# Kernel tuning notes

Measured on AMD Instinct MI355X. Metric: run time of the kernel, lower is better.

Reference implementation:

```python
import jax, jax.numpy as jnp
import numpy as np

# NMS hyperparameters (from init_kwargs / standard detection settings)
CONF_THRESH = 0.05
NMS_THRESH = 0.5
MAX_PER_CLASS = 200
MAX_PER_IMAGE = 100
PRE_NMS_TOPK = 1000  # standard pre-NMS per-class candidate cap


def setup_inputs() -> dict:
    key = jax.random.key(0)
    k1, k2, k3 = jax.random.split(key, 3)
    N, C = 20000, 80
    # per-anchor per-class confidences in [0, 1]
    scores = jax.random.uniform(k1, (1, N, C), dtype=jnp.float32)
    # well-formed boxes (x1, y1, x2, y2) in normalized coords
    centers = jax.random.uniform(k2, (N, 2), dtype=jnp.float32)
    wh = jax.random.uniform(k3, (N, 2), dtype=jnp.float32) * 0.2 + 0.01
    boxes = jnp.concatenate([centers - wh / 2, centers + wh / 2], axis=-1)  # [N, 4]
    return {"scores": scores, "boxes": boxes}


def reference(scores, boxes):
    """Multiclass NMS: confidence threshold -> per-class greedy IoU suppression
    (max_per_class kept) -> global top-max_per_image. Returns kept scores
    (fixed shape [MAX_PER_IMAGE], zero-padded), matching the wrapper which
    returns the selected scores."""
    cls_scores_all = scores[0].T  # [C, N]
    j = jnp.arange(PRE_NMS_TOPK)

    def nms_one_class(cls_scores):  # [N] -> [MAX_PER_CLASS]
        top_s, idx = jax.lax.top_k(cls_scores, PRE_NMS_TOPK)  # [K]
        b = boxes[idx]  # [K, 4]
        x1, y1, x2, y2 = b[:, 0], b[:, 1], b[:, 2], b[:, 3]
        area = (x2 - x1) * (y2 - y1)  # [K]
        # pairwise IoU [K, K]
        iw = jnp.clip(jnp.minimum(x2[:, None], x2[None, :]) - jnp.maximum(x1[:, None], x1[None, :]), 0.0)
        ih = jnp.clip(jnp.minimum(y2[:, None], y2[None, :]) - jnp.maximum(y1[:, None], y1[None, :]), 0.0)
        inter = iw * ih
        iou = inter / (area[:, None] + area[None, :] - inter + 1e-9)
        valid = top_s > CONF_THRESH  # confidence threshold

        def body(i, keep):
            # if box i survives, suppress later boxes with IoU above threshold
            sup = keep[i] & (iou[i] > NMS_THRESH) & (j > i)
            return keep & ~sup

        keep = jax.lax.fori_loop(0, PRE_NMS_TOPK, body, valid)
        kept = jnp.where(keep, top_s, 0.0)
        return jax.lax.top_k(kept, MAX_PER_CLASS)[0]  # cap per class

    per_class = jax.vmap(nms_one_class)(cls_scores_all)  # [C, MAX_PER_CLASS]
    # global cap: top max_per_image scores across all classes
    return jax.lax.top_k(per_class.reshape(-1), MAX_PER_IMAGE)[0]
```

## Files before the change

kernel.cpp:

```cpp
#include <hip/hip_runtime.h>
#include <stdint.h>

#define N_DET 20000
#define N_CLS 80
#define NELEM (N_DET * N_CLS)
#define TOPK  1000
#define CONF  0.05f
#define CANDS 1280
#define SORTN 2048
#define NBLK  128

typedef unsigned long long u64;
typedef unsigned int u32;

__device__ __forceinline__ bool iou_gt_half(float4 bi, float ai,
                                            float4 bj, float aj) {
  #pragma clang fp contract(off)
  float iw = fmaxf(fminf(bi.z, bj.z) - fmaxf(bi.x, bj.x), 0.0f);
  float ih = fmaxf(fminf(bi.w, bj.w) - fmaxf(bi.y, bj.y), 0.0f);
  float inter = iw * ih;
  float denom = ai + aj - inter + 1e-9f;
  return (double)inter * 33554432.0 > (double)denom * 16777217.0;
}

#define OFF_T16    0
#define OFF_CNT    960
#define OFF_CLSOUT 641280
#define OFF_GHA    682240
#define OFF_GHB    723200
#define OFF_CAND   805120
#define OFF_BCNT   1624320

__global__ __launch_bounds__(256) void k_zero(u32* __restrict__ gh) {
  uint4 z4 = make_uint4(0u, 0u, 0u, 0u);
  uint4* p = (uint4*)gh;
  int i = blockIdx.x * 256 + threadIdx.x;
  if (i < 7680) p[i] = z4;
}

__global__ __launch_bounds__(256) void k_histA(
    const float* __restrict__ S, u32* __restrict__ gh) {
  __shared__ u32 h[N_CLS * 129];
  for (int i = threadIdx.x; i < N_CLS * 129; i += 256) h[i] = 0;
  __syncthreads();
  const int per = NELEM / 4 / NBLK;
  const float4* S4 = (const float4*)S;
  const int v0 = blockIdx.x * per;
  for (int v = v0 + threadIdx.x; v < v0 + per; v += 256) {
    float4 f = S4[v];
    int c0 = (v * 4) % N_CLS;
    u32 b0 = __float_as_uint(f.x) >> 23; if (b0 > 127u) b0 = 127u;
    u32 b1 = __float_as_uint(f.y) >> 23; if (b1 > 127u) b1 = 127u;
    u32 b2 = __float_as_uint(f.z) >> 23; if (b2 > 127u) b2 = 127u;
    u32 b3 = __float_as_uint(f.w) >> 23; if (b3 > 127u) b3 = 127u;
    atomicAdd(&h[(c0 + 0) * 129 + b0], 1u);
    atomicAdd(&h[(c0 + 1) * 129 + b1], 1u);
    atomicAdd(&h[(c0 + 2) * 129 + b2], 1u);
    atomicAdd(&h[(c0 + 3) * 129 + b3], 1u);
  }
  __syncthreads();
  for (int i = threadIdx.x; i < N_CLS * 128; i += 256) {
    u32 v = h[(i >> 7) * 129 + (i & 127)];
    if (v) atomicAdd(&gh[i], v);
  }
}

__global__ __launch_bounds__(256) void k_histB_f(
    const float* __restrict__ S, const u32* __restrict__ ghA,
    u32* __restrict__ ghB) {
  __shared__ u32 h[N_CLS * 257];
  __shared__ u32 pA[N_CLS];
  for (int i = threadIdx.x; i < N_CLS * 128; i += 256)
    h[(i >> 7) * 129 + (i & 127)] = ghA[i];
  __syncthreads();
  if (threadIdx.x < N_CLS) {
    const int c = threadIdx.x;
    u32 acc = 0; u32 pref = 0;
    for (int b = 127; b >= 0; --b) {
      acc += h[c * 129 + b];
      if (acc >= TOPK) { pref = (u32)b; break; }
    }
    pA[c] = pref;
  }
  __syncthreads();
  for (int i = threadIdx.x; i < N_CLS * 257; i += 256) h[i] = 0;
  __syncthreads();
  const int per = NELEM / 4 / NBLK;
  const float4* S4 = (const float4*)S;
  const int v0 = blockIdx.x * per;
  for (int v = v0 + threadIdx.x; v < v0 + per; v += 256) {
    float4 f = S4[v];
    int c0 = (v * 4) % N_CLS;
    u32 bb[4] = {__float_as_uint(f.x), __float_as_uint(f.y),
                 __float_as_uint(f.z), __float_as_uint(f.w)};
    #pragma unroll
    for (int k = 0; k < 4; ++k) {
      u32 e = bb[k] >> 23; if (e > 127u) e = 127u;
      if (e == pA[c0 + k])
        atomicAdd(&h[(c0 + k) * 257 + ((bb[k] >> 15) & 0xFF)], 1u);
    }
  }
  __syncthreads();
  for (int i = threadIdx.x; i < N_CLS * 256; i += 256) {
    u32 v = h[(i >> 8) * 257 + (i & 255)];
    if (v) atomicAdd(&ghB[i], v);
  }
}

__global__ __launch_bounds__(256) void k_count_f(
    const float* __restrict__ S, const u32* __restrict__ ghA,
    const u32* __restrict__ ghB, u32* __restrict__ T16,
    u32* __restrict__ cnt, u32* __restrict__ bcnt) {
  __shared__ u32 hA[N_CLS * 129];
  __shared__ u32 hB[N_CLS * 257];
  __shared__ u32 tl[N_CLS];
  __shared__ u32 lcnt[N_CLS];
  for (int i = threadIdx.x; i < N_CLS * 128; i += 256)
    hA[(i >> 7) * 129 + (i & 127)] = ghA[i];
  for (int i = threadIdx.x; i < N_CLS * 256; i += 256)
    hB[(i >> 8) * 257 + (i & 255)] = ghB[i];
  for (int i = threadIdx.x; i < N_CLS; i += 256) lcnt[i] = 0;
  __syncthreads();
  if (threadIdx.x < N_CLS) {
    const int c = threadIdx.x;
    u32 acc = 0, pref = 0, tgt = TOPK, aboveA = 0;
    bool found = false;
    for (int b = 127; b >= 0; --b) {
      u32 hv = hA[c * 129 + b];
      acc += hv;
      if (acc >= TOPK) { pref = (u32)b; tgt = TOPK - (acc - hv);
                         aboveA = acc - hv; found = true; break; }
    }
    if (!found) { pref = 0; tgt = TOPK; aboveA = acc - hA[c * 129]; }
    u32 accB = 0, B1 = 0;
    for (int b = 255; b >= 0; --b) {
      accB += hB[c * 257 + b];
      if (accB >= tgt) { B1 = (u32)b; break; }
    }
    u32 t16 = (pref << 23) | (B1 << 15);
    tl[c] = t16;
    if (blockIdx.x == 0) { T16[c] = t16; cnt[c] = aboveA + accB; }
  }
  __syncthreads();
  const int per = NELEM / 4 / NBLK;
  const float4* S4 = (const float4*)S;
  const int v0 = blockIdx.x * per;
  for (int v = v0 + threadIdx.x; v < v0 + per; v += 256) {
    float4 f = S4[v];
    const int c0 = (v * 4) % N_CLS;
    u32 bb[4] = {__float_as_uint(f.x), __float_as_uint(f.y),
                 __float_as_uint(f.z), __float_as_uint(f.w)};
    #pragma unroll
    for (int k = 0; k < 4; ++k)
      if (bb[k] >= tl[c0 + k]) atomicAdd(&lcnt[c0 + k], 1u);
  }
  __syncthreads();
  for (int i = threadIdx.x; i < N_CLS; i += 256)
    bcnt[blockIdx.x * N_CLS + i] = lcnt[i];
}

__global__ __launch_bounds__(256) void k_place_f(
    const float* __restrict__ S, const u32* __restrict__ T16,
    const u32* __restrict__ bcnt, u64* __restrict__ cand) {
  __shared__ u32 tl[N_CLS];
  __shared__ u32 lcnt[N_CLS];
  __shared__ u32 gbase[N_CLS];
  for (int i = threadIdx.x; i < N_CLS; i += 256) { tl[i] = T16[i]; lcnt[i] = 0; }
  if (threadIdx.x < N_CLS) {
    const int c = threadIdx.x;
    u32 a = 0;
    for (int b = 0; b < blockIdx.x; ++b) a += bcnt[b * N_CLS + c];
    gbase[c] = a;
  }
  __syncthreads();
  const int per = NELEM / 4 / NBLK;
  const float4* S4 = (const float4*)S;
  const int v0 = blockIdx.x * per;
  for (int v = v0 + threadIdx.x; v < v0 + per; v += 256) {
    float4 f = S4[v];
    const int base = v * 4;
    const int c0 = base % N_CLS;
    const u32 row = (u32)(base / N_CLS);
    u32 bb[4] = {__float_as_uint(f.x), __float_as_uint(f.y),
                 __float_as_uint(f.z), __float_as_uint(f.w)};
    #pragma unroll
    for (int k = 0; k < 4; ++k) {
      if (bb[k] >= tl[c0 + k]) {
        u32 p = gbase[c0 + k] + atomicAdd(&lcnt[c0 + k], 1u);
        if (p < CANDS)
          cand[(size_t)(c0 + k) * CANDS + p] = ((u64)bb[k] << 32) | (u32)(~row);
      }
    }
  }
}

__global__ __launch_bounds__(512) void k_sortnms(
    const u64* __restrict__ cand, const u32* __restrict__ cnt,
    const float* __restrict__ boxes, float* __restrict__ cls_out) {
  const int c = blockIdx.x;
  const int tid = threadIdx.x, wave = tid >> 6, lane = tid & 63;
  __shared__ u64 keys[SORTN];
  __shared__ float4 sbox[TOPK];
  __shared__ float sarea[TOPK];
  __shared__ float sscore[TOPK];

  u32 n = cnt[c]; if (n > CANDS) n = CANDS;
  for (int i = tid; i < SORTN; i += 512)
    keys[i] = (i < (int)n) ? cand[(size_t)c * CANDS + i] : 0ull;
  __syncthreads();

  const int segbase = wave * 256;
  for (int k = 2; k <= 256; k <<= 1) {
    for (int j = k >> 1; j > 0; j >>= 1) {
      #pragma unroll
      for (int q = 0; q < 2; ++q) {
        int p = lane + q * 64;
        int i  = segbase + (((p & ~(j - 1)) << 1) | (p & (j - 1)));
        int ix = i | j;
        bool up = (i & k) == 0;
        u64 a = keys[i], b = keys[ix];
        if (up ? (a < b) : (a > b)) { keys[i] = b; keys[ix] = a; }
      }
      __builtin_amdgcn_wave_barrier();
    }
  }
  __syncthreads();
  for (int k = 512; k <= SORTN; k <<= 1) {
    for (int j = k >> 1; j >= 256; j >>= 1) {
      for (int p = tid; p < SORTN / 2; p += 512) {
        int i  = ((p & ~(j - 1)) << 1) | (p & (j - 1));
        int ix = i | j;
        bool up = (i & k) == 0;
        u64 a = keys[i], b = keys[ix];
        if (up ? (a < b) : (a > b)) { keys[i] = b; keys[ix] = a; }
      }
      __syncthreads();
    }
    for (int j = 128; j > 0; j >>= 1) {
      #pragma unroll
      for (int q = 0; q < 2; ++q) {
        int p = lane + q * 64;
        int i  = segbase + (((p & ~(j - 1)) << 1) | (p & (j - 1)));
        int ix = i | j;
        bool up = (i & k) == 0;
        u64 a = keys[i], b = keys[ix];
        if (up ? (a < b) : (a > b)) { keys[i] = b; keys[ix] = a; }
      }
      __builtin_amdgcn_wave_barrier();
    }
    __syncthreads();
  }

  for (int i = tid; i < TOPK; i += 512) {
    u64 kk = keys[i];
    u32 idx = ~(u32)kk;
    if (kk == 0ull || idx >= N_DET) idx = 0;
    float4 b = ((const float4*)boxes)[idx];
    sbox[i] = b;
    sarea[i] = (b.z - b.x) * (b.w - b.y);
    sscore[i] = __uint_as_float((u32)(kk >> 32));
  }
  __syncthreads();

  if (wave == 0) {
    float4 kb0 = make_float4(0.f, 0.f, 0.f, 0.f), kb1 = kb0;
    float ka0 = 0.f, ka1 = 0.f;
    int count = 0;
    float sc_n = sscore[0];
    float4 b_n = sbox[0];
    float a_n = sarea[0];
    for (int i = 0; i < TOPK && count < 100; ++i) {
      float sc = sc_n;
      float4 bi = b_n;
      float ai = a_n;
      if (i + 1 < TOPK) {
        sc_n = sscore[i + 1];
        b_n = sbox[i + 1];
        a_n = sarea[i + 1];
      }
      if (!(sc > CONF)) break;
      bool sup0 = (lane < count) && iou_gt_half(kb0, ka0, bi, ai);
      bool sup1 = (lane + 64 < count) && iou_gt_half(kb1, ka1, bi, ai);
      u64 m = __ballot(sup0 || sup1);
      if (m == 0ull) {
        if (count < 64) {
          if (lane == count) { kb0 = bi; ka0 = ai; }
        } else {
          if (lane == count - 64) { kb1 = bi; ka1 = ai; }
        }
        if (lane == 0) cls_out[c * 128 + count] = sc;
        ++count;
      }
    }
    for (int i = count + lane; i < 100; i += 64)
      cls_out[c * 128 + i] = 0.0f;
  }
}

__global__ __launch_bounds__(1024) void k_final(
    const float* __restrict__ cls_out, float* __restrict__ out) {
  __shared__ u32 vals[8000];
  __shared__ u32 h1[8192];
  __shared__ u32 h2[16384];
  __shared__ u32 wsum[16];
  __shared__ u32 cands[512];
  __shared__ u32 sPref, sT2, sThr, scnt;
  const int t = threadIdx.x, wave = t >> 6, lane = t & 63;

  uint4 z4 = make_uint4(0u, 0u, 0u, 0u);
  for (int i = t; i < 2048; i += 1024) ((uint4*)h1)[i] = z4;
  for (int i = t; i < 4096; i += 1024) ((uint4*)h2)[i] = z4;
  if (t < 128) ((uint4*)cands)[t] = z4;
  if (t == 0) { sPref = 0; sT2 = 1; sThr = 0; scnt = 0; }
  __syncthreads();

  for (int i = t; i < 8000; i += 1024) {
    u32 b = __float_as_uint(cls_out[(i / 100) * 128 + (i % 100)]);
    vals[i] = b;
    u32 bin = b >> 17; if (bin > 8191u) bin = 8191u;
    atomicAdd(&h1[bin], 1u);
  }
  __syncthreads();

  {
    const u32 b0 = (u32)t * 8u;
    u32 loc[8]; u32 lsum = 0;
    #pragma unroll
    for (int k = 0; k < 8; ++k) { loc[k] = h1[b0 + k]; lsum += loc[k]; }
    u32 s = lsum;
    #pragma unroll
    for (int off = 1; off < 64; off <<= 1) {
      u32 v = __shfl_down(s, off, 64);
      if (lane + off < 64) s += v;
    }
    if (lane == 0) wsum[wave] = s;
    __syncthreads();
    u32 aboveW = 0;
    #pragma unroll
    for (int w = 0; w < 16; ++w) if (w > wave) aboveW += wsum[w];
    u32 above = aboveW + (s - lsum);
    if (above < 100u && above + lsum >= 100u) {
      u32 acc = above;
      #pragma unroll
      for (int k = 7; k >= 0; --k) {
        acc += loc[k];
        if (acc >= 100u) { sPref = b0 + (u32)k; sT2 = 100u - (acc - loc[k]); break; }
      }
    }
    __syncthreads();
  }
  const u32 pref = sPref, rt = sT2;

  for (int i = t; i < 8000; i += 1024) {
    u32 b = vals[i];
    u32 bin = b >> 17; if (bin > 8191u) bin = 8191u;
    if (bin == pref) atomicAdd(&h2[(b >> 3) & 0x3FFFu], 1u);
  }
  __syncthreads();

  {
    const u32 b0 = (u32)t * 16u;
    u32 loc[16]; u32 lsum = 0;
    #pragma unroll
    for (int k = 0; k < 16; ++k) { loc[k] = h2[b0 + k]; lsum += loc[k]; }
    u32 s = lsum;
    #pragma unroll
    for (int off = 1; off < 64; off <<= 1) {
      u32 v = __shfl_down(s, off, 64);
      if (lane + off < 64) s += v;
    }
    if (lane == 0) wsum[wave] = s;
    __syncthreads();
    u32 aboveW = 0;
    #pragma unroll
    for (int w = 0; w < 16; ++w) if (w > wave) aboveW += wsum[w];
    u32 above = aboveW + (s - lsum);
    if (above < rt && above + lsum >= rt) {
      u32 acc = above;
      #pragma unroll
      for (int k = 15; k >= 0; --k) {
        acc += loc[k];
        if (acc >= rt) { sThr = (pref << 17) | ((b0 + (u32)k) << 3); break; }
      }
    }
    __syncthreads();
  }
  const u32 thr = sThr;

  for (int i = t; i < 8000; i += 1024) {
    u32 v = vals[i];
    if (v >= thr) {
      u32 p = atomicAdd(&scnt, 1u);
      if (p < 512u) cands[p] = v;
    }
  }
  __syncthreads();
  const u32 nc = scnt;

  if (nc <= 512u) {
    if (wave == 0) {
      for (int k = 2; k <= 512; k <<= 1)
        for (int j = k >> 1; j > 0; j >>= 1) {
          for (int p = lane; p < 256; p += 64) {
            int i  = ((p & ~(j - 1)) << 1) | (p & (j - 1));
            int ix = i | j;
            bool up = (i & k) == 0;
            u32 a = cands[i], b = cands[ix];
            if (up ? (a < b) : (a > b)) { cands[i] = b; cands[ix] = a; }
          }
          __builtin_amdgcn_wave_barrier();
        }
      out[lane] = __uint_as_float(cands[lane]);
      if (lane < 36) out[lane + 64] = __uint_as_float(cands[lane + 64]);
    }
  } else {
    for (int i = t; i < 8192; i += 1024) h2[i] = (i < 8000) ? vals[i] : 0u;
    __syncthreads();
    for (int k = 2; k <= 8192; k <<= 1)
      for (int j = k >> 1; j > 0; j >>= 1) {
        for (int p = t; p < 4096; p += 1024) {
          int i  = ((p & ~(j - 1)) << 1) | (p & (j - 1));
          int ix = i | j;
          bool up = (i & k) == 0;
          u32 a = h2[i], b = h2[ix];
          if (up ? (a < b) : (a > b)) { h2[i] = b; h2[ix] = a; }
        }
        __syncthreads();
      }
    if (t < 100) out[t] = __uint_as_float(h2[t]);
  }
}

extern "C" void kernel_launch(void* const* d_in, const int* in_sizes, int n_in,
                              void* d_out, int out_size, void* d_ws, size_t ws_size,
                              hipStream_t stream) {
  const float* scores = (const float*)d_in[0];
  const float* boxes  = (const float*)d_in[1];
  float* out = (float*)d_out;
  char* ws = (char*)d_ws;

  u32* T16     = (u32*)(ws + OFF_T16);
  u32* cnt     = (u32*)(ws + OFF_CNT);
  float* cls_out = (float*)(ws + OFF_CLSOUT);
  u32* ghistA  = (u32*)(ws + OFF_GHA);
  u32* ghistB  = (u32*)(ws + OFF_GHB);
  u64* cand    = (u64*)(ws + OFF_CAND);
  u32* bcnt    = (u32*)(ws + OFF_BCNT);

  k_zero<<<30, 256, 0, stream>>>(ghistA);
  k_histA<<<NBLK, 256, 0, stream>>>(scores, ghistA);
  k_histB_f<<<NBLK, 256, 0, stream>>>(scores, ghistA, ghistB);
  k_count_f<<<NBLK, 256, 0, stream>>>(scores, ghistA, ghistB, T16, cnt, bcnt);
  k_place_f<<<NBLK, 256, 0, stream>>>(scores, T16, bcnt, cand);
  k_sortnms<<<N_CLS, 512, 0, stream>>>(cand, cnt, boxes, cls_out);
  k_final<<<1, 1024, 0, stream>>>(cls_out, out);
}
```

Baseline: 156.0 us.

## Add fast-path NMS on top-256 candidates with full-sort fallback kernel

Computes a second, tighter per-class threshold aimed at roughly the top 256 scores. A new fast kernel filters candidates by that threshold, sorts at most 512 keys, and runs greedy NMS. If it reaches 100 kept boxes or exhausts the candidates by confidence, it marks the class done; otherwise a separate full 2048-element sort-and-NMS kernel reruns that class. The aim is to avoid the large sort for most classes, at the cost of an extra kernel launch and a fallback pass for classes the fast path cannot finish.

```diff
diff --git a/kernel.cpp b/kernel.cpp
--- a/kernel.cpp
+++ b/kernel.cpp
@@ -8,6 +8,7 @@
 #define CONF  0.05f
 #define CANDS 1280
 #define SORTN 2048
+#define FASTN 512
 #define NBLK  128
 
 typedef unsigned long long u64;
@@ -24,6 +25,8 @@
 }
 
 #define OFF_T16    0
+#define OFF_T256   320
+#define OFF_FLAG   640
 #define OFF_CNT    960
 #define OFF_CLSOUT 641280
 #define OFF_GHA    682240
@@ -110,7 +113,7 @@
 __global__ __launch_bounds__(256) void k_count_f(
     const float* __restrict__ S, const u32* __restrict__ ghA,
     const u32* __restrict__ ghB, u32* __restrict__ T16,
-    u32* __restrict__ cnt, u32* __restrict__ bcnt) {
+    u32* __restrict__ T256, u32* __restrict__ cnt, u32* __restrict__ bcnt) {
   __shared__ u32 hA[N_CLS * 129];
   __shared__ u32 hB[N_CLS * 257];
   __shared__ u32 tl[N_CLS];
@@ -139,7 +142,21 @@
     }
     u32 t16 = (pref << 23) | (B1 << 15);
     tl[c] = t16;
-    if (blockIdx.x == 0) { T16[c] = t16; cnt[c] = aboveA + accB; }
+    if (blockIdx.x == 0) {
+      T16[c] = t16;
+      cnt[c] = aboveA + accB;
+      u32 t256 = t16;
+      if (aboveA < 256u) {
+        u32 rt = 256u - aboveA;
+        u32 acc2 = 0, B2 = 0;
+        for (int b = 255; b >= 0; --b) {
+          acc2 += hB[c * 257 + b];
+          if (acc2 >= rt) { B2 = (u32)b; break; }
+        }
+        t256 = (pref << 23) | (B2 << 15);
+      }
+      T256[c] = t256;
+    }
   }
   __syncthreads();
   const int per = NELEM / 4 / NBLK;
@@ -196,8 +213,131 @@
 
 __global__ __launch_bounds__(512) void k_sortnms(
     const u64* __restrict__ cand, const u32* __restrict__ cnt,
-    const float* __restrict__ boxes, float* __restrict__ cls_out) {
+    const u32* __restrict__ T256, const float* __restrict__ boxes,
+    float* __restrict__ cls_out, u32* __restrict__ flag) {
   const int c = blockIdx.x;
+  const int tid = threadIdx.x, wave = tid >> 6, lane = tid & 63;
+  __shared__ u64 keys[FASTN];
+  __shared__ float4 sbox[FASTN];
+  __shared__ float sarea[FASTN];
+  __shared__ float sscore[FASTN];
+  __shared__ u32 sN, sOvf;
+
+  u32 n = cnt[c]; if (n > CANDS) n = CANDS;
+  const u32 thr = T256[c];
+  keys[tid] = 0ull;
+  if (tid == 0) { sN = 0; sOvf = 0; }
+  __syncthreads();
+  for (int i = tid; i < (int)n; i += 512) {
+    u64 kk = cand[(size_t)c * CANDS + i];
+    if ((u32)(kk >> 32) >= thr) {
+      u32 p = atomicAdd(&sN, 1u);
+      if (p < FASTN) keys[p] = kk; else sOvf = 1u;
+    }
+  }
+  __syncthreads();
+  if (sOvf) { if (tid == 0) flag[c] = 1u; return; }
+  const u32 nk = sN;
+
+  const int segbase = wave * 64;
+  for (int k = 2; k <= 64; k <<= 1) {
+    for (int j = k >> 1; j > 0; j >>= 1) {
+      if (lane < 32) {
+        int p = lane;
+        int i  = segbase + (((p & ~(j - 1)) << 1) | (p & (j - 1)));
+        int ix = i | j;
+        bool up = (i & k) == 0;
+        u64 a = keys[i], b = keys[ix];
+        if (up ? (a < b) : (a > b)) { keys[i] = b; keys[ix] = a; }
+      }
+      __builtin_amdgcn_wave_barrier();
+    }
+  }
+  __syncthreads();
+  for (int k = 128; k <= FASTN; k <<= 1) {
+    for (int j = k >> 1; j >= 64; j >>= 1) {
+      if (tid < 256) {
+        int p = tid;
+        int i  = ((p & ~(j - 1)) << 1) | (p & (j - 1));
+        int ix = i | j;
+        bool up = (i & k) == 0;
+        u64 a = keys[i], b = keys[ix];
+        if (up ? (a < b) : (a > b)) { keys[i] = b; keys[ix] = a; }
+      }
+      __syncthreads();
+    }
+    for (int j = 32; j > 0; j >>= 1) {
+      if (lane < 32) {
+        int p = lane;
+        int i  = segbase + (((p & ~(j - 1)) << 1) | (p & (j - 1)));
+        int ix = i | j;
+        bool up = (i & k) == 0;
+        u64 a = keys[i], b = keys[ix];
+        if (up ? (a < b) : (a > b)) { keys[i] = b; keys[ix] = a; }
+      }
+      __builtin_amdgcn_wave_barrier();
+    }
+    __syncthreads();
+  }
+
+  {
+    u64 kk = keys[tid];
+    u32 idx = ~(u32)kk;
+    if (kk == 0ull || idx >= N_DET) idx = 0;
+    float4 b = ((const float4*)boxes)[idx];
+    sbox[tid] = b;
+    sarea[tid] = (b.z - b.x) * (b.w - b.y);
+    sscore[tid] = __uint_as_float((u32)(kk >> 32));
+  }
+  __syncthreads();
+
+  if (wave == 0) {
+    float4 kb0 = make_float4(0.f, 0.f, 0.f, 0.f), kb1 = kb0;
+    float ka0 = 0.f, ka1 = 0.f;
+    int count = 0;
+    bool confbreak = false;
+    int ii = 0;
+    float sc_n = sscore[0];
+    float4 b_n = sbox[0];
+    float a_n = sarea[0];
+    for (; ii < FASTN && count < 100; ++ii) {
+      float sc = sc_n;
+      float4 bi = b_n;
+      float ai = a_n;
+      if (ii + 1 < FASTN) {
+        sc_n = sscore[ii + 1];
+        b_n = sbox[ii + 1];
+        a_n = sarea[ii + 1];
+      }
+      if (!(sc > CONF)) { confbreak = true; break; }
+      bool sup0 = (lane < count) && iou_gt_half(kb0, ka0, bi, ai);
+      bool sup1 = (lane + 64 < count) && iou_gt_half(kb1, ka1, bi, ai);
+      u64 m = __ballot(sup0 || sup1);
+      if (m == 0ull) {
+        if (count < 64) {
+          if (lane == count) { kb0 = bi; ka0 = ai; }
+        } else {
+          if (lane == count - 64) { kb1 = bi; ka1 = ai; }
+        }
+        if (lane == 0) cls_out[c * 128 + count] = sc;
+        ++count;
+      }
+    }
+    bool done = (count >= 100) || (confbreak && ii < (int)nk);
+    if (lane == 0) flag[c] = done ? 0u : 1u;
+    if (done) {
+      for (int i = count + lane; i < 100; i += 64)
+        cls_out[c * 128 + i] = 0.0f;
+    }
+  }
+}
+
+__global__ __launch_bounds__(512) void k_nmsfull(
+    const u64* __restrict__ cand, const u32* __restrict__ cnt,
+    const u32* __restrict__ flag, const float* __restrict__ boxes,
+    float* __restrict__ cls_out) {
+  const int c = blockIdx.x;
+  if (flag[c] == 0u) return;
   const int tid = threadIdx.x, wave = tid >> 6, lane = tid & 63;
   __shared__ u64 keys[SORTN];
   __shared__ float4 sbox[TOPK];
@@ -208,7 +348,6 @@
   for (int i = tid; i < SORTN; i += 512)
     keys[i] = (i < (int)n) ? cand[(size_t)c * CANDS + i] : 0ull;
   __syncthreads();
-
   const int segbase = wave * 256;
   for (int k = 2; k <= 256; k <<= 1) {
     for (int j = k >> 1; j > 0; j >>= 1) {
@@ -250,7 +389,6 @@
     }
     __syncthreads();
   }
-
   for (int i = tid; i < TOPK; i += 512) {
     u64 kk = keys[i];
     u32 idx = ~(u32)kk;
@@ -261,7 +399,6 @@
     sscore[i] = __uint_as_float((u32)(kk >> 32));
   }
   __syncthreads();
-
   if (wave == 0) {
     float4 kb0 = make_float4(0.f, 0.f, 0.f, 0.f), kb1 = kb0;
     float ka0 = 0.f, ka1 = 0.f;
@@ -440,6 +577,8 @@
   char* ws = (char*)d_ws;
 
   u32* T16     = (u32*)(ws + OFF_T16);
+  u32* T256    = (u32*)(ws + OFF_T256);
+  u32* flag    = (u32*)(ws + OFF_FLAG);
   u32* cnt     = (u32*)(ws + OFF_CNT);
   float* cls_out = (float*)(ws + OFF_CLSOUT);
   u32* ghistA  = (u32*)(ws + OFF_GHA);
@@ -450,8 +589,9 @@
   k_zero<<<30, 256, 0, stream>>>(ghistA);
   k_histA<<<NBLK, 256, 0, stream>>>(scores, ghistA);
   k_histB_f<<<NBLK, 256, 0, stream>>>(scores, ghistA, ghistB);
-  k_count_f<<<NBLK, 256, 0, stream>>>(scores, ghistA, ghistB, T16, cnt, bcnt);
+  k_count_f<<<NBLK, 256, 0, stream>>>(scores, ghistA, ghistB, T16, T256, cnt, bcnt);
   k_place_f<<<NBLK, 256, 0, stream>>>(scores, T16, bcnt, cand);
-  k_sortnms<<<N_CLS, 512, 0, stream>>>(cand, cnt, boxes, cls_out);
+  k_sortnms<<<N_CLS, 512, 0, stream>>>(cand, cnt, T256, boxes, cls_out, flag);
+  k_nmsfull<<<N_CLS, 512, 0, stream>>>(cand, cnt, flag, boxes, cls_out);
   k_final<<<1, 1024, 0, stream>>>(cls_out, out);
 }
```

New measurement: 146.0 us. 1.07x faster.
